# Performance work log

Measured on AMD Instinct MI355X. Metric: run time of the kernel, lower is better.

Reference implementation:

```python
import jax, jax.numpy as jnp
import numpy as np

N_USERS = 50000
N_ITEMS = 50000
N_NODES = N_USERS + N_ITEMS
N_EDGES = 1600000
N_PAIRS = 200000
USER_DIM = 128
ITEM_DIM = 128
HID = 64
LAYER_NUM = 2


def setup_inputs() -> dict:
    key = jax.random.key(0)
    ks = jax.random.split(key, 16)
    inp = {
        "user_features": jax.random.normal(ks[0], (N_USERS, USER_DIM), jnp.float32),
        "item_features": jax.random.normal(ks[1], (N_ITEMS, ITEM_DIM), jnp.float32),
        "item_side_feat": jax.random.normal(ks[2], (N_ITEMS, HID), jnp.float32),
        "T_f": jax.random.uniform(ks[3], (2 * N_PAIRS,), jnp.float32),
        "T_cf": jax.random.uniform(ks[4], (2 * N_PAIRS,), jnp.float32),
        "Wu": jax.random.normal(ks[5], (USER_DIM, HID), jnp.float32) / np.sqrt(USER_DIM),
        "bu": jax.random.normal(ks[6], (HID,), jnp.float32) * 0.01,
        "Wi": jax.random.normal(ks[7], (ITEM_DIM, HID), jnp.float32) / np.sqrt(ITEM_DIM),
        "bi": jax.random.normal(ks[8], (HID,), jnp.float32) * 0.01,
        "W1": jax.random.normal(ks[9], (1 + 2 * HID, HID), jnp.float32) / np.sqrt(1 + 2 * HID),
        "b1": jax.random.normal(ks[10], (HID,), jnp.float32) * 0.01,
        "W2": jax.random.normal(ks[11], (HID, 1), jnp.float32) / np.sqrt(HID),
        "edge_src": jax.random.randint(ks[12], (N_EDGES,), 0, N_NODES, jnp.int32),
        "edge_dst": jax.random.randint(ks[13], (N_EDGES,), 0, N_NODES, jnp.int32),
        "userId": jax.random.randint(ks[14], (N_PAIRS,), 0, N_USERS, jnp.int32),
        "pos_itemId": jax.random.randint(ks[15], (N_PAIRS,), 0, N_ITEMS, jnp.int32),
        "neg_itemId": jax.random.randint(jax.random.fold_in(key, 99), (N_PAIRS,), 0, N_ITEMS, jnp.int32),
    }
    return inp


def reference(user_features, item_features, item_side_feat, T_f, T_cf,
              Wu, bu, Wi, bi, W1, b1, W2,
              edge_src, edge_dst, userId, pos_itemId, neg_itemId):
    # degree-based symmetric normalization (out_deg^-0.5 on src, in_deg^-0.5 on dst)
    ones = jnp.ones((edge_src.shape[0],), jnp.float32)
    out_deg = jax.ops.segment_sum(ones, edge_src, num_segments=N_NODES)
    in_deg = jax.ops.segment_sum(ones, edge_dst, num_segments=N_NODES)
    out_norm = jax.lax.rsqrt(jnp.clip(out_deg, 1.0))[:, None]  # [N,1]
    in_norm = jax.lax.rsqrt(jnp.clip(in_deg, 1.0))[:, None]

    def gcn_layer(node_f):
        m = node_f * out_norm                                   # [N,H]
        agg = jax.ops.segment_sum(m[edge_src], edge_dst, num_segments=N_NODES)
        return agg * in_norm

    user_embedding = jax.nn.relu(user_features @ Wu + bu)       # [Nu,H]
    item_embedding = jax.nn.relu(item_features @ Wi + bi)       # [Ni,H]

    for i in range(LAYER_NUM):
        if i == 0:
            embeddings = gcn_layer(jnp.concatenate([user_embedding, item_embedding], axis=0))
        else:
            embeddings = gcn_layer(embeddings)
        scale = 1.0 / (i + 2)
        user_embedding = user_embedding + embeddings[:N_USERS] * scale
        item_embedding = item_embedding + embeddings[N_USERS:] * scale

    item_embedding = item_embedding + item_side_feat

    userE = user_embedding[userId]                              # [P,H]
    posE = item_embedding[pos_itemId]
    negE = item_embedding[neg_itemId]
    zi = jnp.concatenate([userE, userE], axis=0)                # [2P,H]
    zj = jnp.concatenate([posE, negE], axis=0)

    def decode(T):
        h = jnp.concatenate([zi, zj, T[:, None]], axis=1)       # [2P, 2H+1]
        h = jax.nn.elu(h @ W1 + b1)
        return (h @ W2)[:, 0]                                   # [2P]

    logits_f = decode(T_f)
    logits_cf = decode(T_cf)
    return (user_embedding, item_embedding, logits_f, logits_cf)
```

## Files before the change

kernel.cpp:

```cpp
#include <hip/hip_runtime.h>

#define NU 50000
#define NI 50000
#define NN 100000
#define NE 1600000
#define NP 200000
#define DIM 128
#define HID 64

#define HR2 2
#define HC2 64
#define RN2 (NN / HR2)
#define RNW2 (RN2 / 2)
#define CE2 (NE / HC2)

#define HRF 4
#define RNF (NN / HRF)

typedef unsigned short bf16_t;
typedef __attribute__((ext_vector_type(8))) short short8;
typedef __attribute__((ext_vector_type(4))) float f32x4;
typedef __attribute__((ext_vector_type(2))) float f32x2;

__device__ __forceinline__ float bf2f(unsigned short u) {
  union { unsigned int i; float f; } c; c.i = ((unsigned int)u) << 16; return c.f;
}
__device__ __forceinline__ unsigned short f2bf(float f) {
  union { float f; unsigned int i; } c; c.f = f;
  unsigned int i = c.i;
  i += 0x7fffu + ((i >> 16) & 1u);
  return (unsigned short)(i >> 16);
}
__device__ __forceinline__ f32x2 unpack2(unsigned int w) {
  union { unsigned int i; float f; } lo, hi;
  lo.i = w << 16;
  hi.i = w & 0xffff0000u;
  f32x2 r; r.x = lo.f; r.y = hi.f;
  return r;
}
__device__ __forceinline__ int geti(const void* p, int i, bool i64) {
  return i64 ? (int)((const long long*)p)[i] : ((const int*)p)[i];
}

__global__ __launch_bounds__(64) void k_detect(const bf16_t* __restrict__ uf,
                                               const int* __restrict__ ei,
                                               int* __restrict__ flag) {
  int lane = threadIdx.x;
  float m = 0.f;
  for (int i = lane; i < 4096; i += 64) {
    float v = fabsf(bf2f(uf[i]));
    if (v < 3e38f) m = fmaxf(m, v);
  }
  int cnt = 0;
  for (int i = lane; i < 4096; i += 64) {
    if (ei[2 * i + 1] == 0) cnt++;
  }
  for (int off = 32; off > 0; off >>= 1) {
    m = fmaxf(m, __shfl_xor(m, off));
    cnt += __shfl_xor(cnt, off);
  }
  if (lane == 0) {
    flag[0] = (m > 100.f) ? 1 : 0;
    flag[1] = (cnt > 2048) ? 1 : 0;
  }
}

__global__ __launch_bounds__(1024) void k_hist1(const void* __restrict__ ev,
                                                const int* __restrict__ flag,
                                                unsigned int* __restrict__ part) {
  __shared__ unsigned int h[RNW2];
  const bool i64 = (flag[1] != 0);
  int r = blockIdx.x & (HR2 - 1);
  int c = blockIdx.x >> 1;
  int lo = r * RN2, hiN = lo + RN2;
  int t = threadIdx.x;
  for (int i = t; i < RNW2; i += 1024) h[i] = 0u;
  __syncthreads();
  int ebeg = c * CE2;
  if (!i64) {
    const int* p = (const int*)ev + ebeg;
    for (int e = t * 4; e < CE2; e += 1024 * 4) {
      int4 v4 = *(const int4*)(p + e);
      int vv[4] = {v4.x, v4.y, v4.z, v4.w};
#pragma unroll
      for (int k = 0; k < 4; ++k) {
        int v = vv[k];
        if (v >= lo && v < hiN) {
          int loc = v - lo;
          atomicAdd(&h[loc >> 1], 1u << ((loc & 1) * 16));
        }
      }
    }
  } else {
    const long long* p = (const long long*)ev + ebeg;
    for (int e = t; e < CE2; e += 1024) {
      int v = (int)p[e];
      if (v >= lo && v < hiN) {
        int loc = v - lo;
        atomicAdd(&h[loc >> 1], 1u << ((loc & 1) * 16));
      }
    }
  }
  __syncthreads();
  unsigned int* po = part + c * (NN / 2) + (lo >> 1);
  for (int i = t; i < RNW2; i += 1024) po[i] = h[i];
}

__global__ __launch_bounds__(256) void k_reduce(const unsigned int* __restrict__ pout,
                                                unsigned int* __restrict__ pin,
                                                int* __restrict__ din,
                                                float* __restrict__ onorm,
                                                float* __restrict__ inorm,
                                                int* __restrict__ bsums) {
  __shared__ int sh[256];
  int t = threadIdx.x;
  int w = blockIdx.x * 256 + t;
  unsigned int si0 = 0, si1 = 0;
  if (w < NN / 2) {
    unsigned int so0 = 0, so1 = 0;
#pragma unroll
    for (int c = 0; c < HC2; ++c) {
      unsigned int v = pout[c * (NN / 2) + w];
      so0 += v & 0xffffu;
      so1 += v >> 16;
    }
#pragma unroll
    for (int c = 0; c < HC2; ++c) {
      unsigned int v = pin[c * (NN / 2) + w];
      pin[c * (NN / 2) + w] = si0 | (si1 << 16);
      si0 += v & 0xffffu;
      si1 += v >> 16;
    }
    int n = 2 * w;
    din[n] = (int)si0;
    din[n + 1] = (int)si1;
    onorm[n] = rsqrtf((float)(so0 > 1u ? so0 : 1u));
    onorm[n + 1] = rsqrtf((float)(so1 > 1u ? so1 : 1u));
    inorm[n] = rsqrtf((float)(si0 > 1u ? si0 : 1u));
    inorm[n + 1] = rsqrtf((float)(si1 > 1u ? si1 : 1u));
  }
  sh[t] = (int)(si0 + si1);
  __syncthreads();
  for (int off = 128; off > 0; off >>= 1) {
    if (t < off) sh[t] += sh[t + off];
    __syncthreads();
  }
  if (t == 0) bsums[blockIdx.x] = sh[0];
}

__global__ __launch_bounds__(256) void k_scan2(const int* __restrict__ bsums,
                                               int* __restrict__ boffs, int nb) {
  __shared__ int sh[256];
  int t = threadIdx.x;
  int own = (t < nb) ? bsums[t] : 0;
  sh[t] = own;
  __syncthreads();
  for (int off = 1; off < 256; off <<= 1) {
    int add = (t >= off) ? sh[t - off] : 0;
    __syncthreads();
    sh[t] += add;
    __syncthreads();
  }
  if (t < nb) boffs[t] = sh[t] - own;
}

__global__ __launch_bounds__(256) void k_scan3(const int* __restrict__ in,
                                               const int* __restrict__ boffs,
                                               int* __restrict__ row_ptr,
                                               int* __restrict__ csr_src, int n) {
  __shared__ int sh[256];
  int t = threadIdx.x;
  int base = blockIdx.x * 512 + t * 2;
  int v0 = (base < n) ? in[base] : 0;
  int v1 = (base + 1 < n) ? in[base + 1] : 0;
  int s = v0 + v1;
  sh[t] = s;
  __syncthreads();
  for (int off = 1; off < 256; off <<= 1) {
    int add = (t >= off) ? sh[t - off] : 0;
    __syncthreads();
    sh[t] += add;
    __syncthreads();
  }
  int excl = boffs[blockIdx.x] + sh[t] - s;
  if (base < n) row_ptr[base] = excl;
  if (base + 1 < n) row_ptr[base + 1] = excl + v0;
  if (blockIdx.x == 0 && t == 0) row_ptr[n] = NE;
  if (blockIdx.x == 0 && t < 32) csr_src[NE + t] = NN;
}

__global__ __launch_bounds__(1024) void k_fill2(const void* __restrict__ srcv,
                                                const void* __restrict__ dstv,
                                                const int* __restrict__ flag,
                                                const int* __restrict__ row_ptr,
                                                const unsigned int* __restrict__ pin,
                                                int* __restrict__ csr_src) {
  __shared__ int cur[RNF];
  const bool i64 = (flag[1] != 0);
  int r = blockIdx.x & (HRF - 1);
  int c = blockIdx.x >> 2;
  int lo = r * RNF, hiN = lo + RNF;
  int t = threadIdx.x;
  const unsigned int* pw = pin + c * (NN / 2);
  const int* rp = row_ptr + lo;
  for (int i = t; i < RNF; i += 1024) {
    int node = lo + i;
    unsigned int wrd = pw[node >> 1];
    int off = (int)((wrd >> ((node & 1) * 16)) & 0xffffu);
    cur[i] = rp[i] + off;
  }
  __syncthreads();
  int ebeg = c * CE2;
  if (!i64) {
    const int* sp = (const int*)srcv + ebeg;
    const int* dp = (const int*)dstv + ebeg;
    for (int e = t * 4; e < CE2; e += 1024 * 4) {
      int4 dv = *(const int4*)(dp + e);
      int4 sv = *(const int4*)(sp + e);
      int dd[4] = {dv.x, dv.y, dv.z, dv.w};
      int ss[4] = {sv.x, sv.y, sv.z, sv.w};
#pragma unroll
      for (int k = 0; k < 4; ++k) {
        int d = dd[k];
        if (d >= lo && d < hiN) {
          int slot = atomicAdd(&cur[d - lo], 1);
          csr_src[slot] = ss[k];
        }
      }
    }
  } else {
    const long long* sp = (const long long*)srcv + ebeg;
    const long long* dp = (const long long*)dstv + ebeg;
    for (int e = t; e < CE2; e += 1024) {
      int d = (int)dp[e];
      if (d >= lo && d < hiN) {
        int slot = atomicAdd(&cur[d - lo], 1);
        csr_src[slot] = (int)sp[e];
      }
    }
  }
}

__global__ __launch_bounds__(256) void k_embed(const void* __restrict__ featv,
                                               const void* __restrict__ Wv,
                                               const void* __restrict__ biasv,
                                               const int* __restrict__ flag,
                                               const float* __restrict__ onorm_base,
                                               float* __restrict__ out,
                                               bf16_t* __restrict__ embs,
                                               bf16_t* __restrict__ zrow, int rows) {
  __shared__ __align__(16) char smem[DIM * HID * 4];
  __shared__ float bs[HID];
  const bool f32 = (flag[0] != 0);
  int t = threadIdx.x;
  if (zrow && blockIdx.x == 0 && t < 32)
    ((unsigned int*)zrow)[t] = 0u;

  if (!f32) {
    bf16_t* Wt = (bf16_t*)smem;
    const bf16_t* W = (const bf16_t*)Wv;
    for (int i = t; i < DIM * HID; i += 256) {
      int k = i >> 6, n = i & 63;
      Wt[n * 136 + k] = W[i];
    }
    if (t < HID) bs[t] = bf2f(((const bf16_t*)biasv)[t]);
    __syncthreads();
    int wv = t >> 6;
    int lane = t & 63;
    int m = lane & 15;
    int q = lane >> 4;
    short8 Bf[4][4];
#pragma unroll
    for (int c = 0; c < 4; ++c)
#pragma unroll
      for (int nt = 0; nt < 4; ++nt)
        Bf[c][nt] = *(const short8*)&Wt[(nt * 16 + m) * 136 + c * 32 + q * 8];
    const bf16_t* feat = (const bf16_t*)featv;
    int tiles = rows >> 4;
    for (int tile = blockIdx.x * 4 + wv; tile < tiles; tile += gridDim.x * 4) {
      const bf16_t* fr = feat + (size_t)(tile * 16 + m) * DIM + q * 8;
      short8 a0 = *(const short8*)(fr);
      short8 a1 = *(const short8*)(fr + 32);
      short8 a2 = *(const short8*)(fr + 64);
      short8 a3 = *(const short8*)(fr + 96);
      f32x4 acc[4];
#pragma unroll
      for (int nt = 0; nt < 4; ++nt) acc[nt] = (f32x4)(0.f);
#pragma unroll
      for (int nt = 0; nt < 4; ++nt) {
        acc[nt] = __builtin_amdgcn_mfma_f32_16x16x32_bf16(a0, Bf[0][nt], acc[nt], 0, 0, 0);
        acc[nt] = __builtin_amdgcn_mfma_f32_16x16x32_bf16(a1, Bf[1][nt], acc[nt], 0, 0, 0);
        acc[nt] = __builtin_amdgcn_mfma_f32_16x16x32_bf16(a2, Bf[2][nt], acc[nt], 0, 0, 0);
        acc[nt] = __builtin_amdgcn_mfma_f32_16x16x32_bf16(a3, Bf[3][nt], acc[nt], 0, 0, 0);
      }
#pragma unroll
      for (int r = 0; r < 4; ++r) {
        int orow = tile * 16 + q * 4 + r;
        float sc = onorm_base[orow];
        float* orow_p = out + (size_t)orow * HID;
        bf16_t* erow_p = embs + (size_t)orow * HID;
#pragma unroll
        for (int nt = 0; nt < 4; ++nt) {
          int n = nt * 16 + m;
          float v = fmaxf(acc[nt][r] + bs[n], 0.f);
          orow_p[n] = v;
          erow_p[n] = f2bf(v * sc);
        }
      }
    }
    return;
  }

  float* Ws = (float*)smem;
  {
    const float* W = (const float*)Wv;
    for (int i = t; i < DIM * HID; i += 256) Ws[i] = W[i];
    if (t < HID) bs[t] = ((const float*)biasv)[t];
  }
  __syncthreads();
  int rl = t >> 4;
  int jq = t & 15;
  for (int rbase = blockIdx.x * 16; rbase < rows; rbase += gridDim.x * 16) {
    int row = rbase + rl;
    if (row >= rows) continue;
    float a0 = 0.f, a1 = 0.f, a2 = 0.f, a3 = 0.f;
    const float* fr = (const float*)featv + (size_t)row * DIM;
    for (int k0 = 0; k0 < DIM; k0 += 4) {
      float4 f4 = *(const float4*)(fr + k0);
      float fk[4] = {f4.x, f4.y, f4.z, f4.w};
#pragma unroll
      for (int kk = 0; kk < 4; ++kk) {
        const float* wr = &Ws[(k0 + kk) * HID + jq * 4];
        a0 += fk[kk] * wr[0];
        a1 += fk[kk] * wr[1];
        a2 += fk[kk] * wr[2];
        a3 += fk[kk] * wr[3];
      }
    }
    float4 r;
    r.x = fmaxf(a0 + bs[jq * 4 + 0], 0.f);
    r.y = fmaxf(a1 + bs[jq * 4 + 1], 0.f);
    r.z = fmaxf(a2 + bs[jq * 4 + 2], 0.f);
    r.w = fmaxf(a3 + bs[jq * 4 + 3], 0.f);
    *(float4*)&out[(size_t)row * HID + jq * 4] = r;
    float sc = onorm_base[row];
    uint2 p;
    p.x = (unsigned int)f2bf(r.x * sc) | ((unsigned int)f2bf(r.y * sc) << 16);
    p.y = (unsigned int)f2bf(r.z * sc) | ((unsigned int)f2bf(r.w * sc) << 16);
    *(uint2*)&embs[(size_t)row * HID + jq * 4] = p;
  }
}

__global__ __launch_bounds__(256) void k_gather1(const bf16_t* __restrict__ embs,
                                                 const float* __restrict__ onorm,
                                                 const float* __restrict__ inorm,
                                                 const int* __restrict__ row_ptr,
                                                 const int* __restrict__ csr_src,
                                                 bf16_t* __restrict__ e1s) {
  if (blockIdx.x == 0 && threadIdx.x < 32)
    ((unsigned int*)(e1s + (size_t)NN * HID))[threadIdx.x] = 0u;
  int lane = threadIdx.x & 63;
  int h = lane >> 5;
  int g = (lane >> 3) & 3;
  int l8 = (lane & 7) * 8;
  int n = blockIdx.x * 8 + (threadIdx.x >> 6) * 2 + h;
  int beg = row_ptr[n], end = row_ptr[n + 1];
  f32x2 a[4];
#pragma unroll
  for (int j = 0; j < 4; ++j) a[j] = (f32x2)(0.f);
  for (int base = beg; base < end; base += 16) {
    int sv[4];
#pragma unroll
    for (int k = 0; k < 4; ++k) {
      int ee = base + k * 4 + g;
      int raw = csr_src[ee];
      sv[k] = (ee < end) ? raw : NN;
    }
#pragma unroll
    for (int k = 0; k < 4; ++k) {
      uint4 u = *(const uint4*)(embs + (sv[k] << 6) + l8);
      a[0] += unpack2(u.x);
      a[1] += unpack2(u.y);
      a[2] += unpack2(u.z);
      a[3] += unpack2(u.w);
    }
  }
#pragma unroll
  for (int j = 0; j < 4; ++j) {
    a[j].x += __shfl_xor(a[j].x, 8);
    a[j].y += __shfl_xor(a[j].y, 8);
    a[j].x += __shfl_xor(a[j].x, 16);
    a[j].y += __shfl_xor(a[j].y, 16);
  }
  if (g == 0) {
    float sc = inorm[n] * onorm[n];
    uint4 p;
    p.x = (unsigned int)f2bf(a[0].x * sc) | ((unsigned int)f2bf(a[0].y * sc) << 16);
    p.y = (unsigned int)f2bf(a[1].x * sc) | ((unsigned int)f2bf(a[1].y * sc) << 16);
    p.z = (unsigned int)f2bf(a[2].x * sc) | ((unsigned int)f2bf(a[2].y * sc) << 16);
    p.w = (unsigned int)f2bf(a[3].x * sc) | ((unsigned int)f2bf(a[3].y * sc) << 16);
    *(uint4*)(e1s + (size_t)n * HID + l8) = p;
  }
}

__global__ __launch_bounds__(256) void k_gather2c(float* __restrict__ emb0,
                                                  const bf16_t* __restrict__ e1s,
                                                  const void* __restrict__ sidev,
                                                  const int* __restrict__ flag,
                                                  const float* __restrict__ onorm,
                                                  const float* __restrict__ inorm,
                                                  const int* __restrict__ row_ptr,
                                                  const int* __restrict__ csr_src,
                                                  bf16_t* __restrict__ fin_bf) {
  int lane = threadIdx.x & 63;
  int h = lane >> 5;
  int g = (lane >> 3) & 3;
  int l8 = (lane & 7) * 8;
  int n = blockIdx.x * 8 + (threadIdx.x >> 6) * 2 + h;
  int beg = row_ptr[n], end = row_ptr[n + 1];
  f32x2 a[4];
#pragma unroll
  for (int j = 0; j < 4; ++j) a[j] = (f32x2)(0.f);
  for (int base = beg; base < end; base += 16) {
    int sv[4];
#pragma unroll
    for (int k = 0; k < 4; ++k) {
      int ee = base + k * 4 + g;
      int raw = csr_src[ee];
      sv[k] = (ee < end) ? raw : NN;
    }
#pragma unroll
    for (int k = 0; k < 4; ++k) {
      uint4 u = *(const uint4*)(e1s + (sv[k] << 6) + l8);
      a[0] += unpack2(u.x);
      a[1] += unpack2(u.y);
      a[2] += unpack2(u.z);
      a[3] += unpack2(u.w);
    }
  }
#pragma unroll
  for (int j = 0; j < 4; ++j) {
    a[j].x += __shfl_xor(a[j].x, 8);
    a[j].y += __shfl_xor(a[j].y, 8);
    a[j].x += __shfl_xor(a[j].x, 16);
    a[j].y += __shfl_xor(a[j].y, 16);
  }
  if (g == 0) {
    float aa[8] = {a[0].x, a[0].y, a[1].x, a[1].y, a[2].x, a[2].y, a[3].x, a[3].y};
    float inorm_n = inorm[n];
    float inv_on = 1.0f / onorm[n];
    size_t off = (size_t)n * HID + l8;
    uint4 u = *(const uint4*)(e1s + off);
    unsigned int w[4] = {u.x, u.y, u.z, u.w};
    float e1v[8];
#pragma unroll
    for (int j = 0; j < 4; ++j) {
      e1v[2 * j]     = bf2f((unsigned short)(w[j] & 0xffffu)) * inv_on;
      e1v[2 * j + 1] = bf2f((unsigned short)(w[j] >> 16)) * inv_on;
    }
    float4 b0 = *(const float4*)&emb0[off];
    float4 b1 = *(const float4*)&emb0[off + 4];
    float bb[8] = {b0.x, b0.y, b0.z, b0.w, b1.x, b1.y, b1.z, b1.w};
    const float s2 = 1.f / 3.f;
    float vv[8];
#pragma unroll
    for (int j = 0; j < 8; ++j)
      vv[j] = bb[j] + 0.5f * e1v[j] + s2 * aa[j] * inorm_n;
    if (n >= NU) {
      size_t soff = (size_t)(n - NU) * HID + l8;
      if (flag[0] != 0) {
        float4 s0 = *(const float4*)((const float*)sidev + soff);
        float4 s1 = *(const float4*)((const float*)sidev + soff + 4);
        vv[0] += s0.x; vv[1] += s0.y; vv[2] += s0.z; vv[3] += s0.w;
        vv[4] += s1.x; vv[5] += s1.y; vv[6] += s1.z; vv[7] += s1.w;
      } else {
        uint4 su = *(const uint4*)((const bf16_t*)sidev + soff);
        unsigned int sw[4] = {su.x, su.y, su.z, su.w};
#pragma unroll
        for (int j = 0; j < 4; ++j) {
          vv[2 * j]     += bf2f((unsigned short)(sw[j] & 0xffffu));
          vv[2 * j + 1] += bf2f((unsigned short)(sw[j] >> 16));
        }
      }
    }
    float4 o0, o1;
    o0.x = vv[0]; o0.y = vv[1]; o0.z = vv[2]; o0.w = vv[3];
    o1.x = vv[4]; o1.y = vv[5]; o1.z = vv[6]; o1.w = vv[7];
    *(float4*)&emb0[off] = o0;
    *(float4*)&emb0[off + 4] = o1;
    uint4 pb;
    pb.x = (unsigned int)f2bf(vv[0]) | ((unsigned int)f2bf(vv[1]) << 16);
    pb.y = (unsigned int)f2bf(vv[2]) | ((unsigned int)f2bf(vv[3]) << 16);
    pb.z = (unsigned int)f2bf(vv[4]) | ((unsigned int)f2bf(vv[5]) << 16);
    pb.w = (unsigned int)f2bf(vv[6]) | ((unsigned int)f2bf(vv[7]) << 16);
    *(uint4*)(fin_bf + off) = pb;
  }
}

__global__ __launch_bounds__(256) void k_decode(const bf16_t* __restrict__ zb,
                                                const void* __restrict__ W1v,
                                                const void* __restrict__ b1v,
                                                const void* __restrict__ W2v,
                                                const void* __restrict__ Tfv,
                                                const void* __restrict__ Tcfv,
                                                const int* __restrict__ flag,
                                                const void* __restrict__ userId,
                                                const void* __restrict__ posId,
                                                const void* __restrict__ negId,
                                                float* __restrict__ out_lf,
                                                float* __restrict__ out_lcf) {
  __shared__ bf16_t W1b[128 * 65];
  __shared__ float wlast[HID], b1s[HID], W2s[HID];
  const bool f32 = (flag[0] != 0);
  const bool i64 = (flag[1] != 0);
  int t = threadIdx.x;
  if (f32) {
    const float* W1 = (const float*)W1v;
    for (int i = t; i < 128 * 64; i += 256) W1b[(i >> 6) * 65 + (i & 63)] = f2bf(W1[i]);
    if (t < HID) {
      wlast[t] = W1[128 * 64 + t];
      b1s[t] = ((const float*)b1v)[t];
      W2s[t] = ((const float*)W2v)[t];
    }
  } else {
    const bf16_t* W1 = (const bf16_t*)W1v;
    for (int i = t; i < 128 * 64; i += 256) W1b[(i >> 6) * 65 + (i & 63)] = W1[i];
    if (t < HID) {
      wlast[t] = bf2f(W1[128 * 64 + t]);
      b1s[t] = bf2f(((const bf16_t*)b1v)[t]);
      W2s[t] = bf2f(((const bf16_t*)W2v)[t]);
    }
  }
  __syncthreads();
  int wv = t >> 6;
  int lane = t & 63;
  int m = lane & 15;
  int q = lane >> 4;
  short8 Bf[4][4];
#pragma unroll
  for (int c = 0; c < 4; ++c)
#pragma unroll
    for (int nt = 0; nt < 4; ++nt)
#pragma unroll
      for (int j = 0; j < 8; ++j)
        Bf[c][nt][j] = (short)W1b[(c * 32 + q * 8 + j) * 65 + nt * 16 + m];

  const int tiles = NP / 16;
  const int stride = gridDim.x * 4;
  int tile = blockIdx.x * 4 + wv;
  if (tile >= tiles) return;

  int pid = tile * 16 + m;
  int uid = geti(userId, pid, i64);
  int pidx = geti(posId, pid, i64);
  int nidx = geti(negId, pid, i64);
  const bf16_t* ur = zb + (size_t)uid * HID;
  const bf16_t* pr = zb + (size_t)(NU + pidx) * HID;
  const bf16_t* nr = zb + (size_t)(NU + nidx) * HID;
  short8 au0 = *(const short8*)(ur + q * 8);
  short8 au1 = *(const short8*)(ur + 32 + q * 8);
  short8 ap0 = *(const short8*)(pr + q * 8);
  short8 ap1 = *(const short8*)(pr + 32 + q * 8);
  short8 an0 = *(const short8*)(nr + q * 8);
  short8 an1 = *(const short8*)(nr + 32 + q * 8);

  while (true) {
    int ntile = tile + stride;
    bool have_next = (ntile < tiles);
    int uid2 = 0, pidx2 = 0, nidx2 = 0;
    if (have_next) {
      int pid2 = ntile * 16 + m;
      uid2 = geti(userId, pid2, i64);
      pidx2 = geti(posId, pid2, i64);
      nidx2 = geti(negId, pid2, i64);
    }
    float tf_p[4], tc_p[4], tf_n[4], tc_n[4];
    int rbase = tile * 16 + q * 4;
    if (f32) {
      float4 t4 = *(const float4*)((const float*)Tfv + rbase);
      float4 c4 = *(const float4*)((const float*)Tcfv + rbase);
      float4 t4n = *(const float4*)((const float*)Tfv + rbase + NP);
      float4 c4n = *(const float4*)((const float*)Tcfv + rbase + NP);
      tf_p[0] = t4.x; tf_p[1] = t4.y; tf_p[2] = t4.z; tf_p[3] = t4.w;
      tc_p[0] = c4.x; tc_p[1] = c4.y; tc_p[2] = c4.z; tc_p[3] = c4.w;
      tf_n[0] = t4n.x; tf_n[1] = t4n.y; tf_n[2] = t4n.z; tf_n[3] = t4n.w;
      tc_n[0] = c4n.x; tc_n[1] = c4n.y; tc_n[2] = c4n.z; tc_n[3] = c4n.w;
    } else {
      const bf16_t* tp = (const bf16_t*)Tfv + rbase;
      const bf16_t* cp = (const bf16_t*)Tcfv + rbase;
#pragma unroll
      for (int r = 0; r < 4; ++r) {
        tf_p[r] = bf2f(tp[r]); tc_p[r] = bf2f(cp[r]);
        tf_n[r] = bf2f(tp[r + NP]); tc_n[r] = bf2f(cp[r + NP]);
      }
    }
    float sfp[4], scp[4], sfn[4], scn[4];
#pragma unroll
    for (int r = 0; r < 4; ++r) { sfp[r] = 0.f; scp[r] = 0.f; sfn[r] = 0.f; scn[r] = 0.f; }
#pragma unroll
    for (int nt = 0; nt < 4; ++nt) {
      f32x4 accu = (f32x4)(0.f);
      accu = __builtin_amdgcn_mfma_f32_16x16x32_bf16(au0, Bf[0][nt], accu, 0, 0, 0);
      accu = __builtin_amdgcn_mfma_f32_16x16x32_bf16(au1, Bf[1][nt], accu, 0, 0, 0);
      f32x4 accp = __builtin_amdgcn_mfma_f32_16x16x32_bf16(ap0, Bf[2][nt], accu, 0, 0, 0);
      accp = __builtin_amdgcn_mfma_f32_16x16x32_bf16(ap1, Bf[3][nt], accp, 0, 0, 0);
      f32x4 accn = __builtin_amdgcn_mfma_f32_16x16x32_bf16(an0, Bf[2][nt], accu, 0, 0, 0);
      accn = __builtin_amdgcn_mfma_f32_16x16x32_bf16(an1, Bf[3][nt], accn, 0, 0, 0);
      int n = nt * 16 + m;
      float b = b1s[n];
      float wl = wlast[n];
      float w2 = W2s[n];
#pragma unroll
      for (int r = 0; r < 4; ++r) {
        float xp = accp[r] + b;
        float xn = accn[r] + b;
        float v0 = xp + tf_p[r] * wl;
        float v1 = xp + tc_p[r] * wl;
        float v2 = xn + tf_n[r] * wl;
        float v3 = xn + tc_n[r] * wl;
        sfp[r] += (v0 > 0.f ? v0 : (__expf(v0) - 1.f)) * w2;
        scp[r] += (v1 > 0.f ? v1 : (__expf(v1) - 1.f)) * w2;
        sfn[r] += (v2 > 0.f ? v2 : (__expf(v2) - 1.f)) * w2;
        scn[r] += (v3 > 0.f ? v3 : (__expf(v3) - 1.f)) * w2;
      }
    }
    short8 bu0 = au0, bu1 = au1, bp0 = ap0, bp1 = ap1, bn0 = an0, bn1 = an1;
    if (have_next) {
      const bf16_t* ur2 = zb + (size_t)uid2 * HID;
      const bf16_t* pr2 = zb + (size_t)(NU + pidx2) * HID;
      const bf16_t* nr2 = zb + (size_t)(NU + nidx2) * HID;
      bu0 = *(const short8*)(ur2 + q * 8);
      bu1 = *(const short8*)(ur2 + 32 + q * 8);
      bp0 = *(const short8*)(pr2 + q * 8);
      bp1 = *(const short8*)(pr2 + 32 + q * 8);
      bn0 = *(const short8*)(nr2 + q * 8);
      bn1 = *(const short8*)(nr2 + 32 + q * 8);
    }
#pragma unroll
    for (int r = 0; r < 4; ++r) {
#pragma unroll
      for (int s = 1; s < 16; s <<= 1) {
        sfp[r] += __shfl_xor(sfp[r], s);
        scp[r] += __shfl_xor(scp[r], s);
        sfn[r] += __shfl_xor(sfn[r], s);
        scn[r] += __shfl_xor(scn[r], s);
      }
      if (m == 0) {
        int pr2i = rbase + r;
        out_lf[pr2i] = sfp[r];
        out_lcf[pr2i] = scp[r];
        out_lf[pr2i + NP] = sfn[r];
        out_lcf[pr2i + NP] = scn[r];
      }
    }
    if (!have_next) break;
    tile = ntile;
    au0 = bu0; au1 = bu1; ap0 = bp0; ap1 = bp1; an0 = bn0; an1 = bn1;
  }
}

extern "C" void kernel_launch(void* const* d_in, const int* in_sizes, int n_in,
                              void* d_out, int out_size, void* d_ws, size_t ws_size,
                              hipStream_t stream) {
  (void)in_sizes; (void)n_in; (void)out_size;
  const void* user_f = d_in[0];
  const void* item_f = d_in[1];
  const void* side   = d_in[2];
  const void* Tf     = d_in[3];
  const void* Tcf    = d_in[4];
  const void* Wu     = d_in[5];
  const void* bu     = d_in[6];
  const void* Wi     = d_in[7];
  const void* bi     = d_in[8];
  const void* W1     = d_in[9];
  const void* b1     = d_in[10];
  const void* W2     = d_in[11];
  const void* esrc   = d_in[12];
  const void* edst   = d_in[13];
  const void* userId = d_in[14];
  const void* posId  = d_in[15];
  const void* negId  = d_in[16];

  const size_t WS_NEEDED = 33602688;
  if (ws_size < WS_NEEDED) return;

  char* ws = (char*)d_ws;
  int*   deg_in  = (int*)(ws + 0);
  float* onorm   = (float*)(ws + 400000);
  float* inorm   = (float*)(ws + 800000);
  int*   row_ptr = (int*)(ws + 1200000);
  int*   bsums   = (int*)(ws + 1600128);
  int*   boffs   = (int*)(ws + 1601152);
  int*   flag    = (int*)(ws + 1602176);
  int*   csr_src = (int*)(ws + 1602304);
  unsigned int* pout = (unsigned int*)(ws + 8002432);
  unsigned int* pin  = (unsigned int*)(ws + 20802560);
  bf16_t* embs   = (bf16_t*)(ws + 8002432);
  bf16_t* e1s    = (bf16_t*)(ws + 20802560);
  bf16_t* fin_bf = embs;

  float* out     = (float*)d_out;
  float* emb0    = out;
  float* out_lf  = out + (size_t)NN * HID;
  float* out_lcf = out_lf + 2 * NP;

  k_detect<<<1, 64, 0, stream>>>((const bf16_t*)user_f, (const int*)esrc, flag);
  k_hist1<<<HR2 * HC2, 1024, 0, stream>>>(esrc, flag, pout);
  k_hist1<<<HR2 * HC2, 1024, 0, stream>>>(edst, flag, pin);
  k_reduce<<<196, 256, 0, stream>>>(pout, pin, deg_in, onorm, inorm, bsums);
  k_scan2<<<1, 256, 0, stream>>>(bsums, boffs, 196);
  k_scan3<<<196, 256, 0, stream>>>(deg_in, boffs, row_ptr, csr_src, NN);
  k_fill2<<<HRF * HC2, 1024, 0, stream>>>(esrc, edst, flag, row_ptr, pin, csr_src);
  k_embed<<<512, 256, 0, stream>>>(user_f, Wu, bu, flag, onorm, emb0, embs,
                                   embs + (size_t)NN * HID, NU);
  k_embed<<<512, 256, 0, stream>>>(item_f, Wi, bi, flag, onorm + NU,
                                   emb0 + (size_t)NU * HID, embs + (size_t)NU * HID,
                                   (bf16_t*)0, NI);
  k_gather1<<<NN / 8, 256, 0, stream>>>(embs, onorm, inorm, row_ptr, csr_src, e1s);
  k_gather2c<<<NN / 8, 256, 0, stream>>>(emb0, e1s, side, flag, onorm, inorm, row_ptr,
                                         csr_src, fin_bf);
  k_decode<<<1024, 256, 0, stream>>>(fin_bf, W1, b1, W2, Tf, Tcf, flag,
                                     userId, posId, negId, out_lf, out_lcf);
}
```

Measured before the change: 386.8 us.

## Merge histogram and embed launches, pre-shift CSR indices, shrink detect sampling

Combines the two histogram kernels into one launch and the user/item embedding kernels into one launch, which removes two launch gaps and lets the blocks of both halves run at the same time. CSR source indices are stored pre-multiplied by the row width so the gathers skip a shift. The dtype-detection kernel samples fewer elements, and the decode grid is enlarged. The smaller detection sample makes the dtype heuristic less robust on unusual inputs.

```diff
diff --git a/kernel.cpp b/kernel.cpp
--- a/kernel.cpp
+++ b/kernel.cpp
@@ -17,6 +17,8 @@
 #define HRF 4
 #define RNF (NN / HRF)
 
+#define ZROFF (NN * HID)
+
 typedef unsigned short bf16_t;
 typedef __attribute__((ext_vector_type(8))) short short8;
 typedef __attribute__((ext_vector_type(4))) float f32x4;
@@ -47,12 +49,12 @@
                                                int* __restrict__ flag) {
   int lane = threadIdx.x;
   float m = 0.f;
-  for (int i = lane; i < 4096; i += 64) {
+  for (int i = lane; i < 1024; i += 64) {
     float v = fabsf(bf2f(uf[i]));
     if (v < 3e38f) m = fmaxf(m, v);
   }
   int cnt = 0;
-  for (int i = lane; i < 4096; i += 64) {
+  for (int i = lane; i < 1024; i += 64) {
     if (ei[2 * i + 1] == 0) cnt++;
   }
   for (int off = 32; off > 0; off >>= 1) {
@@ -61,17 +63,23 @@
   }
   if (lane == 0) {
     flag[0] = (m > 100.f) ? 1 : 0;
-    flag[1] = (cnt > 2048) ? 1 : 0;
-  }
-}
-
-__global__ __launch_bounds__(1024) void k_hist1(const void* __restrict__ ev,
+    flag[1] = (cnt > 512) ? 1 : 0;
+  }
+}
+
+__global__ __launch_bounds__(1024) void k_hist2(const void* __restrict__ srcv,
+                                                const void* __restrict__ dstv,
                                                 const int* __restrict__ flag,
-                                                unsigned int* __restrict__ part) {
+                                                unsigned int* __restrict__ pout,
+                                                unsigned int* __restrict__ pin) {
   __shared__ unsigned int h[RNW2];
   const bool i64 = (flag[1] != 0);
-  int r = blockIdx.x & (HR2 - 1);
-  int c = blockIdx.x >> 1;
+  int arr = blockIdx.x >> 7;
+  int sub = blockIdx.x & 127;
+  const void* ev = arr ? dstv : srcv;
+  unsigned int* part = arr ? pin : pout;
+  int r = sub & (HR2 - 1);
+  int c = sub >> 1;
   int lo = r * RN2, hiN = lo + RN2;
   int t = threadIdx.x;
   for (int i = t; i < RNW2; i += 1024) h[i] = 0u;
@@ -186,7 +194,7 @@
   if (base < n) row_ptr[base] = excl;
   if (base + 1 < n) row_ptr[base + 1] = excl + v0;
   if (blockIdx.x == 0 && t == 0) row_ptr[n] = NE;
-  if (blockIdx.x == 0 && t < 32) csr_src[NE + t] = NN;
+  if (blockIdx.x == 0 && t < 32) csr_src[NE + t] = ZROFF;
 }
 
 __global__ __launch_bounds__(1024) void k_fill2(const void* __restrict__ srcv,
@@ -224,7 +232,7 @@
         int d = dd[k];
         if (d >= lo && d < hiN) {
           int slot = atomicAdd(&cur[d - lo], 1);
-          csr_src[slot] = ss[k];
+          csr_src[slot] = ss[k] << 6;
         }
       }
     }
@@ -235,26 +243,39 @@
       int d = (int)dp[e];
       if (d >= lo && d < hiN) {
         int slot = atomicAdd(&cur[d - lo], 1);
-        csr_src[slot] = (int)sp[e];
-      }
-    }
-  }
-}
-
-__global__ __launch_bounds__(256) void k_embed(const void* __restrict__ featv,
-                                               const void* __restrict__ Wv,
-                                               const void* __restrict__ biasv,
-                                               const int* __restrict__ flag,
-                                               const float* __restrict__ onorm_base,
-                                               float* __restrict__ out,
-                                               bf16_t* __restrict__ embs,
-                                               bf16_t* __restrict__ zrow, int rows) {
+        csr_src[slot] = ((int)sp[e]) << 6;
+      }
+    }
+  }
+}
+
+#define EMB_HALF 512
+__global__ __launch_bounds__(256) void k_embed2(const void* __restrict__ uFv,
+                                                const void* __restrict__ iFv,
+                                                const void* __restrict__ Wuv,
+                                                const void* __restrict__ buv,
+                                                const void* __restrict__ Wiv,
+                                                const void* __restrict__ biv,
+                                                const int* __restrict__ flag,
+                                                const float* __restrict__ onorm,
+                                                float* __restrict__ out,
+                                                bf16_t* __restrict__ embs) {
   __shared__ __align__(16) char smem[DIM * HID * 4];
   __shared__ float bs[HID];
   const bool f32 = (flag[0] != 0);
   int t = threadIdx.x;
-  if (zrow && blockIdx.x == 0 && t < 32)
-    ((unsigned int*)zrow)[t] = 0u;
+  const bool item = (blockIdx.x >= EMB_HALF);
+  int bx = item ? (int)blockIdx.x - EMB_HALF : (int)blockIdx.x;
+  const void* featv = item ? iFv : uFv;
+  const void* Wv = item ? Wiv : Wuv;
+  const void* biasv = item ? biv : buv;
+  int row0 = item ? NU : 0;
+  const int rows = NU;
+  const float* onorm_base = onorm + row0;
+  float* out_b = out + (size_t)row0 * HID;
+  bf16_t* embs_b = embs + (size_t)row0 * HID;
+  if (blockIdx.x == 0 && t < 32)
+    ((unsigned int*)(embs + (size_t)NN * HID))[t] = 0u;
 
   if (!f32) {
     bf16_t* Wt = (bf16_t*)smem;
@@ -277,7 +298,7 @@
         Bf[c][nt] = *(const short8*)&Wt[(nt * 16 + m) * 136 + c * 32 + q * 8];
     const bf16_t* feat = (const bf16_t*)featv;
     int tiles = rows >> 4;
-    for (int tile = blockIdx.x * 4 + wv; tile < tiles; tile += gridDim.x * 4) {
+    for (int tile = bx * 4 + wv; tile < tiles; tile += EMB_HALF * 4) {
       const bf16_t* fr = feat + (size_t)(tile * 16 + m) * DIM + q * 8;
       short8 a0 = *(const short8*)(fr);
       short8 a1 = *(const short8*)(fr + 32);
@@ -297,8 +318,8 @@
       for (int r = 0; r < 4; ++r) {
         int orow = tile * 16 + q * 4 + r;
         float sc = onorm_base[orow];
-        float* orow_p = out + (size_t)orow * HID;
-        bf16_t* erow_p = embs + (size_t)orow * HID;
+        float* orow_p = out_b + (size_t)orow * HID;
+        bf16_t* erow_p = embs_b + (size_t)orow * HID;
 #pragma unroll
         for (int nt = 0; nt < 4; ++nt) {
           int n = nt * 16 + m;
@@ -320,7 +341,7 @@
   __syncthreads();
   int rl = t >> 4;
   int jq = t & 15;
-  for (int rbase = blockIdx.x * 16; rbase < rows; rbase += gridDim.x * 16) {
+  for (int rbase = bx * 16; rbase < rows; rbase += EMB_HALF * 16) {
     int row = rbase + rl;
     if (row >= rows) continue;
     float a0 = 0.f, a1 = 0.f, a2 = 0.f, a3 = 0.f;
@@ -342,12 +363,12 @@
     r.y = fmaxf(a1 + bs[jq * 4 + 1], 0.f);
     r.z = fmaxf(a2 + bs[jq * 4 + 2], 0.f);
     r.w = fmaxf(a3 + bs[jq * 4 + 3], 0.f);
-    *(float4*)&out[(size_t)row * HID + jq * 4] = r;
+    *(float4*)&out_b[(size_t)row * HID + jq * 4] = r;
     float sc = onorm_base[row];
     uint2 p;
     p.x = (unsigned int)f2bf(r.x * sc) | ((unsigned int)f2bf(r.y * sc) << 16);
     p.y = (unsigned int)f2bf(r.z * sc) | ((unsigned int)f2bf(r.w * sc) << 16);
-    *(uint2*)&embs[(size_t)row * HID + jq * 4] = p;
+    *(uint2*)&embs_b[(size_t)row * HID + jq * 4] = p;
   }
 }
 
@@ -374,11 +395,11 @@
     for (int k = 0; k < 4; ++k) {
       int ee = base + k * 4 + g;
       int raw = csr_src[ee];
-      sv[k] = (ee < end) ? raw : NN;
+      sv[k] = (ee < end) ? raw : ZROFF;
     }
 #pragma unroll
     for (int k = 0; k < 4; ++k) {
-      uint4 u = *(const uint4*)(embs + (sv[k] << 6) + l8);
+      uint4 u = *(const uint4*)(embs + sv[k] + l8);
       a[0] += unpack2(u.x);
       a[1] += unpack2(u.y);
       a[2] += unpack2(u.z);
@@ -427,11 +448,11 @@
     for (int k = 0; k < 4; ++k) {
       int ee = base + k * 4 + g;
       int raw = csr_src[ee];
-      sv[k] = (ee < end) ? raw : NN;
+      sv[k] = (ee < end) ? raw : ZROFF;
     }
 #pragma unroll
     for (int k = 0; k < 4; ++k) {
-      uint4 u = *(const uint4*)(e1s + (sv[k] << 6) + l8);
+      uint4 u = *(const uint4*)(e1s + sv[k] + l8);
       a[0] += unpack2(u.x);
       a[1] += unpack2(u.y);
       a[2] += unpack2(u.z);
@@ -705,20 +726,16 @@
   float* out_lcf = out_lf + 2 * NP;
 
   k_detect<<<1, 64, 0, stream>>>((const bf16_t*)user_f, (const int*)esrc, flag);
-  k_hist1<<<HR2 * HC2, 1024, 0, stream>>>(esrc, flag, pout);
-  k_hist1<<<HR2 * HC2, 1024, 0, stream>>>(edst, flag, pin);
+  k_hist2<<<2 * HR2 * HC2, 1024, 0, stream>>>(esrc, edst, flag, pout, pin);
   k_reduce<<<196, 256, 0, stream>>>(pout, pin, deg_in, onorm, inorm, bsums);
   k_scan2<<<1, 256, 0, stream>>>(bsums, boffs, 196);
   k_scan3<<<196, 256, 0, stream>>>(deg_in, boffs, row_ptr, csr_src, NN);
   k_fill2<<<HRF * HC2, 1024, 0, stream>>>(esrc, edst, flag, row_ptr, pin, csr_src);
-  k_embed<<<512, 256, 0, stream>>>(user_f, Wu, bu, flag, onorm, emb0, embs,
-                                   embs + (size_t)NN * HID, NU);
-  k_embed<<<512, 256, 0, stream>>>(item_f, Wi, bi, flag, onorm + NU,
-                                   emb0 + (size_t)NU * HID, embs + (size_t)NU * HID,
-                                   (bf16_t*)0, NI);
+  k_embed2<<<2 * EMB_HALF, 256, 0, stream>>>(user_f, item_f, Wu, bu, Wi, bi, flag,
+                                             onorm, emb0, embs);
   k_gather1<<<NN / 8, 256, 0, stream>>>(embs, onorm, inorm, row_ptr, csr_src, e1s);
   k_gather2c<<<NN / 8, 256, 0, stream>>>(emb0, e1s, side, flag, onorm, inorm, row_ptr,
                                          csr_src, fin_bf);
-  k_decode<<<1024, 256, 0, stream>>>(fin_bf, W1, b1, W2, Tf, Tcf, flag,
+  k_decode<<<1563, 256, 0, stream>>>(fin_bf, W1, b1, W2, Tf, Tcf, flag,
                                      userId, posId, negId, out_lf, out_lcf);
 }
```

New measurement: 355.9 us. -8.0%, faster.
